# Optimization experiments

Measured on AMD Instinct MI355X. Metric: run time of the kernel, lower is better.

The kernel has to match this reference:

```python
import jax, jax.numpy as jnp
import numpy as np

D = 256        # d_model
NH = 8         # num_head
NL = 4         # num_level
KS = 8         # kernel_size (even)
K2 = KS * KS
HD = D // NH   # head_dim
LEVELS = [(128, 128), (64, 64), (32, 32), (16, 16)]


def _kernel_indices():
    # even kernel: linspace(-KS/2+0.5, KS/2-0.5, KS), meshgrid ij, stack [j,i] (x,y), / KS
    idx = np.linspace(-KS // 2 + 0.5, KS // 2 - 0.5, KS).astype(np.float32)
    i, j = np.meshgrid(idx, idx, indexing='ij')
    return jnp.asarray(np.stack([j, i], axis=-1).reshape(-1, 2) / KS)  # [K2, 2]


def setup_inputs():
    key = jax.random.key(0)
    ks = jax.random.split(key, 12)
    b, q = 2, 300
    l2 = sum(h * w for h, w in LEVELS)
    query = jax.random.normal(ks[0], (b, q, D), jnp.float32)
    value = jax.random.normal(ks[1], (b, l2, D), jnp.float32)
    v_shape = np.array(LEVELS, dtype=np.int64)                      # [NL, 2] (H, W)
    starts = np.concatenate([[0], np.cumsum([h * w for h, w in LEVELS])[:-1]])
    v_start_index = starts.astype(np.int64)                          # [NL]
    v_mask = jnp.zeros((b, l2), dtype=bool)                          # no padding
    v_valid_ratios = jnp.ones((b, 1, 1, NL, 1, 2), jnp.float32)
    center = jax.random.uniform(ks[2], (b, q, 2), jnp.float32, 0.25, 0.75)
    size = jax.random.uniform(ks[3], (b, q, 2), jnp.float32, 0.05, 0.25)
    ref_windows = jnp.concatenate([center, size], axis=-1)           # [b, q, 4] cx,cy,w,h
    s = 0.02
    Wv = s * jax.random.normal(ks[4], (D, D), jnp.float32)
    bv = jnp.zeros((D,), jnp.float32)
    Wbox = s * jax.random.normal(ks[5], (NH * NL * 4, D), jnp.float32)
    bbox = jax.random.uniform(ks[6], (NH * NL * 4,), jnp.float32)    # uniform init per _reset_parameters
    Wattn = s * jax.random.normal(ks[7], (NH * NL * 4, D), jnp.float32)
    battn = s * jax.random.normal(ks[8], (NH * NL * 4,), jnp.float32)
    Wout = s * jax.random.normal(ks[9], (D, D), jnp.float32)
    bout = jnp.zeros((D,), jnp.float32)
    return dict(query=query, value=value, v_shape=v_shape, v_mask=v_mask,
                v_start_index=v_start_index, v_valid_ratios=v_valid_ratios,
                ref_windows=ref_windows, Wv=Wv, bv=bv, Wbox=Wbox, bbox=bbox,
                Wattn=Wattn, battn=battn, Wout=Wout, bout=bout,
                kernel_indices=_kernel_indices())


def reference(query, value, v_shape, v_mask, v_start_index, v_valid_ratios,
              ref_windows, Wv, bv, Wbox, bbox, Wattn, battn, Wout, bout,
              kernel_indices):
    b, q, _ = query.shape
    # value projection + mask fill
    val = jnp.einsum('bnd,ed->bne', value, Wv) + bv
    val = jnp.where(v_mask[..., None], 0.0, val)
    val = val.reshape(b, -1, NH, HD)                                 # [b, l2, NH, HD]

    # attention logits: base 2x2 grid expanded to KSxKS via repeat_interleave
    aw = (jnp.einsum('bqd,od->bqo', query, Wattn) + battn).reshape(b, q, NH, NL, 2, 2)
    aw = jnp.repeat(jnp.repeat(aw, KS // 2, axis=-1), KS // 2, axis=-2)  # [b,q,NH,NL,KS,KS]
    spatial = jax.nn.softmax(aw.reshape(b, q, NH, NL * K2), axis=-1).reshape(b, q, NH, NL, K2)
    level = jax.nn.softmax(aw, axis=3).reshape(b, q, NH, NL, K2)

    # sampling grid (_where_to_attend)
    ob = (jnp.einsum('bqd,od->bqo', query, Wbox) + bbox).reshape(b, q, NH, NL, 4)
    rw = ref_windows[:, :, None, None, :]                            # [b,q,1,1,4]
    boxes = rw + ob / 8.0 * rw[..., jnp.array([2, 3, 2, 3])]
    center = boxes[..., None, :2]                                    # [b,q,NH,NL,1,2]
    size = boxes[..., None, 2:]
    grid = center + kernel_indices * jax.nn.relu(size)               # [b,q,NH,NL,K2,2]
    grid = grid * v_valid_ratios

    # multi-level bilinear sampling (grid_sample, align_corners=False, zero padding)
    bi = jnp.arange(b)[:, None, None, None]
    hi = jnp.arange(NH)[None, None, :, None]
    sampled = []
    for lv in range(NL):
        Hl = int(v_shape[lv, 0]); Wl = int(v_shape[lv, 1]); st = int(v_start_index[lv])
        vl = val[:, st:st + Hl * Wl]                                 # [b, Hl*Wl, NH, HD]
        loc = grid[:, :, :, lv]                                      # [b,q,NH,K2,2]
        x = loc[..., 0] * Wl - 0.5
        y = loc[..., 1] * Hl - 0.5
        x0 = jnp.floor(x); y0 = jnp.floor(y)
        dx = x - x0; dy = y - y0
        acc = jnp.zeros((b, q, NH, K2, HD), val.dtype)
        for ix, iy, w in ((x0, y0, (1 - dx) * (1 - dy)),
                          (x0 + 1, y0, dx * (1 - dy)),
                          (x0, y0 + 1, (1 - dx) * dy),
                          (x0 + 1, y0 + 1, dx * dy)):
            valid = (ix >= 0) & (ix < Wl) & (iy >= 0) & (iy < Hl)
            idx = (jnp.clip(iy, 0, Hl - 1) * Wl + jnp.clip(ix, 0, Wl - 1)).astype(jnp.int32)
            v4 = vl[bi, idx, hi]                                     # [b,q,NH,K2,HD]
            acc = acc + jnp.where(valid, w, 0.0)[..., None] * v4
        sampled.append(acc)
    sampled = jnp.stack(sampled, axis=3)                             # [b,q,NH,NL,K2,HD]

    # box-attention output: spatial softmax over all (level, point)
    out = jnp.einsum('bqhlkd,bqhlk->bqhd', sampled, spatial).reshape(b, q, D)
    out = jnp.einsum('bqd,od->bqo', out, Wout) + bout
    # instance mask output: level softmax per kernel point
    mask = jnp.einsum('bqhlkd,bqhlk->bqkhd', sampled, level).reshape(b, q, K2, D)
    mask = jnp.einsum('bqkd,od->bqko', mask, Wout) + bout
    return out, mask
```

## Files before the change

kernel.cpp:

```cpp
#include <hip/hip_runtime.h>
#include <cstdint>
#include <cstddef>

typedef unsigned short u16;
typedef unsigned int   u32;
typedef __attribute__((ext_vector_type(8))) short bf16x8;
typedef __attribute__((ext_vector_type(4))) float f32x4;

static constexpr int kQ = 300;
static constexpr int kL2 = 21760;

__device__ __forceinline__ u16 bf16_rne(float f) {
    u32 u = __float_as_uint(f);
    u += 0x7FFFu + ((u >> 16) & 1u);
    return (u16)(u >> 16);
}
__device__ __forceinline__ u32 pack2(float lo, float hi) {
    return (u32)bf16_rne(lo) | ((u32)bf16_rne(hi) << 16);
}
__device__ __forceinline__ float lo16(u32 u) { return __uint_as_float(u << 16); }
__device__ __forceinline__ float hi16(u32 u) { return __uint_as_float(u & 0xFFFF0000u); }

__global__ __launch_bounds__(256)
void f32_to_bf16(const float* __restrict__ src, u16* __restrict__ dst, int n)
{
    int i = (blockIdx.x * 256 + threadIdx.x) * 8;
    if (i >= n) return;
    float4 a = *(const float4*)(src + i);
    float4 b = *(const float4*)(src + i + 4);
    uint4 o;
    o.x = pack2(a.x, a.y); o.y = pack2(a.z, a.w);
    o.z = pack2(b.x, b.y); o.w = pack2(b.z, b.w);
    *(uint4*)(dst + i) = o;
}

template<bool OUT_BF16>
__global__ __launch_bounds__(256)
void gemm_bf16(const u16* __restrict__ A, const u16* __restrict__ W,
               const float* __restrict__ bias, void* __restrict__ Cout,
               const unsigned char* __restrict__ rowmask)
{
    __shared__ u16 S[8192];
    u16* As = S;
    u16* Bs = S + 4096;
    const int tid = threadIdx.x;
    const int m0 = blockIdx.x * 128;
    const int n0 = blockIdx.y * 128;
    const int lane = tid & 63;
    const int w = tid >> 6;
    const int wm = w & 1, wn = w >> 1;
    const int g = lane >> 4, r = lane & 15;

    f32x4 acc[4][4];
#pragma unroll
    for (int i = 0; i < 4; i++)
#pragma unroll
        for (int j = 0; j < 4; j++)
            acc[i][j] = (f32x4){0.f, 0.f, 0.f, 0.f};

    for (int kt = 0; kt < 8; ++kt) {
        const int k0 = kt * 32;
#pragma unroll
        for (int i = 0; i < 2; ++i) {
            int c = tid + i * 256;
            int m = c >> 2, gg = c & 3;
            uint4 va = *(const uint4*)(A + (size_t)(m0 + m) * 256 + k0 + gg * 8);
            *(uint4*)(As + ((gg * 128 + m) << 3)) = va;
            uint4 vb = *(const uint4*)(W + (size_t)(n0 + m) * 256 + k0 + gg * 8);
            *(uint4*)(Bs + ((gg * 128 + m) << 3)) = vb;
        }
        __syncthreads();
        bf16x8 af[4], bf[4];
#pragma unroll
        for (int mf = 0; mf < 4; ++mf)
            af[mf] = *(const bf16x8*)(As + ((g * 128 + wm * 64 + mf * 16 + r) << 3));
#pragma unroll
        for (int nf = 0; nf < 4; ++nf)
            bf[nf] = *(const bf16x8*)(Bs + ((g * 128 + wn * 64 + nf * 16 + r) << 3));
#pragma unroll
        for (int mf = 0; mf < 4; ++mf)
#pragma unroll
            for (int nf = 0; nf < 4; ++nf)
                acc[mf][nf] = __builtin_amdgcn_mfma_f32_16x16x32_bf16(
                    af[mf], bf[nf], acc[mf][nf], 0, 0, 0);
        __syncthreads();
    }

    if (!OUT_BF16) {
        float* C = (float*)Cout;
#pragma unroll
        for (int nf = 0; nf < 4; ++nf) {
            int ng = n0 + wn * 64 + nf * 16 + r;
            float bb = bias[ng];
#pragma unroll
            for (int mf = 0; mf < 4; ++mf) {
                int mg = m0 + wm * 64 + mf * 16 + g * 4;
#pragma unroll
                for (int reg = 0; reg < 4; ++reg) {
                    float z = 1.f;
                    if (rowmask && rowmask[mg + reg]) z = 0.f;
                    C[(size_t)(mg + reg) * 256 + ng] = (acc[mf][nf][reg] + bb) * z;
                }
            }
        }
    } else {
        u16* C = (u16*)Cout;
#pragma unroll
        for (int round = 0; round < 2; ++round) {
            __syncthreads();
            if (wn == round) {
#pragma unroll
                for (int nf = 0; nf < 4; ++nf) {
                    int col = nf * 16 + r;
                    float bb = bias[n0 + round * 64 + col];
#pragma unroll
                    for (int mf = 0; mf < 4; ++mf) {
                        int row0 = wm * 64 + mf * 16 + g * 4;
#pragma unroll
                        for (int reg = 0; reg < 4; ++reg) {
                            float z = 1.f;
                            if (rowmask && rowmask[m0 + row0 + reg]) z = 0.f;
                            S[(row0 + reg) * 64 + col] =
                                bf16_rne((acc[mf][nf][reg] + bb) * z);
                        }
                    }
                }
            }
            __syncthreads();
            int row = tid >> 1, hb = tid & 1;
            const u16* src = S + row * 64 + hb * 32;
            u16* dst = C + (size_t)(m0 + row) * 256 + n0 + round * 64 + hb * 32;
#pragma unroll
            for (int j = 0; j < 4; ++j)
                ((uint4*)dst)[j] = ((const uint4*)src)[j];
        }
    }
}

__global__ __launch_bounds__(256)
void gemm_nt_bias(const float* __restrict__ A, const float* __restrict__ W,
                  const float* __restrict__ bias, float* __restrict__ C, int M)
{
    __shared__ float As[32][68];
    __shared__ float Ws[32][68];
    const int tid = threadIdx.x;
    const int m0 = blockIdx.x * 64;
    const int n0 = blockIdx.y * 64;
    const int tx = tid & 15, ty = tid >> 4;
    float acc[4][4] = {};

    for (int k0 = 0; k0 < 256; k0 += 32) {
#pragma unroll
        for (int i = 0; i < 2; i++) {
            int t = tid + i * 256;
            int rr = t >> 3;
            int c4 = (t & 7) << 2;
            int ra = min(m0 + rr, M - 1);
            float4 va = *(const float4*)(A + (size_t)ra * 256 + k0 + c4);
            As[c4 + 0][rr] = va.x; As[c4 + 1][rr] = va.y;
            As[c4 + 2][rr] = va.z; As[c4 + 3][rr] = va.w;
            float4 vw = *(const float4*)(W + (size_t)(n0 + rr) * 256 + k0 + c4);
            Ws[c4 + 0][rr] = vw.x; Ws[c4 + 1][rr] = vw.y;
            Ws[c4 + 2][rr] = vw.z; Ws[c4 + 3][rr] = vw.w;
        }
        __syncthreads();
#pragma unroll
        for (int kk = 0; kk < 32; kk++) {
            float4 a = *(const float4*)&As[kk][ty * 4];
            float4 wv4 = *(const float4*)&Ws[kk][tx * 4];
            float av[4] = {a.x, a.y, a.z, a.w};
            float wv[4] = {wv4.x, wv4.y, wv4.z, wv4.w};
#pragma unroll
            for (int i = 0; i < 4; i++)
#pragma unroll
                for (int j = 0; j < 4; j++)
                    acc[i][j] += av[i] * wv[j];
        }
        __syncthreads();
    }
#pragma unroll
    for (int i = 0; i < 4; i++) {
        int rr = m0 + ty * 4 + i;
        if (rr >= M) continue;
        int n = n0 + tx * 4;
        float4 o;
        o.x = acc[i][0] + bias[n + 0];
        o.y = acc[i][1] + bias[n + 1];
        o.z = acc[i][2] + bias[n + 2];
        o.w = acc[i][3] + bias[n + 3];
        *(float4*)(C + (size_t)rr * 256 + n) = o;
    }
}

__global__ __launch_bounds__(256)
void param_kernel(const float* __restrict__ query,
                  const float* __restrict__ Wattn, const float* __restrict__ battn,
                  const float* __restrict__ Wbox,  const float* __restrict__ bbox,
                  const float* __restrict__ ref_windows,
                  const float* __restrict__ vvr,
                  float* __restrict__ params)
{
    __shared__ float qrow[256];
    __shared__ float awob[256];
    __shared__ float4 boxs[8][4];
    __shared__ float wgts[8][4][4];
    __shared__ float cqds[8][4];

    const int bq = blockIdx.x;
    const int b = bq / kQ;
    const int tid = threadIdx.x;

    if (tid < 64)
        ((float4*)qrow)[tid] = ((const float4*)(query + (size_t)bq * 256))[tid];
    __syncthreads();

    {
        const float* Wrow = (tid < 128) ? (Wattn + (size_t)tid * 256)
                                        : (Wbox + (size_t)(tid - 128) * 256);
        float s = (tid < 128) ? battn[tid] : bbox[tid - 128];
#pragma unroll 8
        for (int d4 = 0; d4 < 64; d4++) {
            float4 wv = ((const float4*)Wrow)[d4];
            float4 qv = ((const float4*)qrow)[d4];
            s += wv.x * qv.x + wv.y * qv.y + wv.z * qv.z + wv.w * qv.w;
        }
        awob[tid] = s;
    }
    __syncthreads();

    if (tid < 8) {
        const int h = tid;
        float m = -1e30f;
        float E[16];
#pragma unroll
        for (int i = 0; i < 16; i++) m = fmaxf(m, awob[h * 16 + i]);
        float Ssum = 0.f;
#pragma unroll
        for (int i = 0; i < 16; i++) { E[i] = expf(awob[h * 16 + i] - m); Ssum += E[i]; }
        float invS16 = 1.f / (16.f * Ssum);
#pragma unroll
        for (int qd = 0; qd < 4; qd++) {
            float Sq = E[qd] + E[4 + qd] + E[8 + qd] + E[12 + qd];
            float inv = 1.f / Sq;
#pragma unroll
            for (int l = 0; l < 4; l++) wgts[h][l][qd] = E[l * 4 + qd] * inv;
            cqds[h][qd] = Sq * invS16;
        }
    }
    if (tid >= 64 && tid < 96) {
        const int t = tid - 64;
        const int h = t >> 2, l = t & 3;
        float4 rw = ((const float4*)ref_windows)[bq];
        float ob0 = awob[128 + h * 16 + l * 4 + 0];
        float ob1 = awob[128 + h * 16 + l * 4 + 1];
        float ob2 = awob[128 + h * 16 + l * 4 + 2];
        float ob3 = awob[128 + h * 16 + l * 4 + 3];
        float cx = rw.x + ob0 * 0.125f * rw.z;
        float cy = rw.y + ob1 * 0.125f * rw.w;
        float sx = fmaxf(rw.z + ob2 * 0.125f * rw.z, 0.f);
        float sy = fmaxf(rw.w + ob3 * 0.125f * rw.w, 0.f);
        float vrx = vvr[(b * 4 + l) * 2 + 0];
        float vry = vvr[(b * 4 + l) * 2 + 1];
        boxs[h][l] = make_float4(cx * vrx, cy * vry, sx * vrx, sy * vry);
    }
    __syncthreads();

    float* p = params + (size_t)bq * 288;
    if (tid < 32)       ((float4*)p)[tid] = ((float4*)boxs)[tid];
    else if (tid < 64)  ((float4*)p)[tid] = ((float4*)wgts)[tid - 32];
    else if (tid < 72)  ((float4*)p)[tid] = ((float4*)cqds)[tid - 64];
}

__global__ __launch_bounds__(512)
void sample_bf16(const u16* __restrict__ valb,
                 const float* __restrict__ params,
                 u16* __restrict__ maskb,
                 float* __restrict__ out_part)
{
    __shared__ float4 boxs[8][4];
    __shared__ float wgts[8][4][4];
    __shared__ float cqds[8][4];
    __shared__ float warr[8][256];

    const int blk = blockIdx.x;
    const int bq = blk >> 2;
    const int kq = blk & 3;
    const int b = bq / kQ;
    const int tid = threadIdx.x;

    if (tid < 72) {
        float4 v = ((const float4*)(params + (size_t)bq * 288))[tid];
        if (tid < 32)      ((float4*)boxs)[tid] = v;
        else if (tid < 64) ((float4*)wgts)[tid - 32] = v;
        else               ((float4*)cqds)[tid - 64] = v;
    }
    __syncthreads();

    const int klocal = tid >> 5;
    const int h = (tid >> 2) & 7;
    const int ch = tid & 3;
    const int k = kq * 16 + klocal;
    const float kx = (float)(k & 7) * 0.125f - 0.4375f;
    const float ky = (float)(k >> 3) * 0.125f - 0.4375f;
    const int qd = (((k >> 5) & 1) << 1) | ((k >> 2) & 1);

    float acc[8];
#pragma unroll
    for (int e = 0; e < 8; e++) acc[e] = 0.f;

    static constexpr int LW[4]  = {128, 64, 32, 16};
    static constexpr int LST[4] = {0, 16384, 20480, 21504};

#pragma unroll
    for (int l = 0; l < 4; l++) {
        const int Wl = LW[l];
        const u16* vbase = valb + ((size_t)(b * kL2 + LST[l]) << 8) + h * 32 + ch * 8;
        float4 bx = boxs[h][l];
        float lw = wgts[h][l][qd];
        float x = (bx.x + kx * bx.z) * Wl - 0.5f;
        float y = (bx.y + ky * bx.w) * Wl - 0.5f;
        float x0f = floorf(x), y0f = floorf(y);
        float dx = x - x0f, dy = y - y0f;
        int x0 = (int)x0f, y0 = (int)y0f;
        int x1 = x0 + 1, y1 = y0 + 1;
        int x0c = min(max(x0, 0), Wl - 1), x1c = min(max(x1, 0), Wl - 1);
        int y0c = min(max(y0, 0), Wl - 1), y1c = min(max(y1, 0), Wl - 1);
        float vx0 = (x0 >= 0 && x0 < Wl) ? 1.f : 0.f;
        float vx1 = (x1 >= 0 && x1 < Wl) ? 1.f : 0.f;
        float vy0 = (y0 >= 0 && y0 < Wl) ? 1.f : 0.f;
        float vy1 = (y1 >= 0 && y1 < Wl) ? 1.f : 0.f;
        float w00 = (1.f - dx) * (1.f - dy) * vx0 * vy0 * lw;
        float w10 = dx * (1.f - dy) * vx1 * vy0 * lw;
        float w01 = (1.f - dx) * dy * vx0 * vy1 * lw;
        float w11 = dx * dy * vx1 * vy1 * lw;
        uint4 v00 = *(const uint4*)(vbase + ((size_t)(y0c * Wl + x0c) << 8));
        uint4 v10 = *(const uint4*)(vbase + ((size_t)(y0c * Wl + x1c) << 8));
        uint4 v01 = *(const uint4*)(vbase + ((size_t)(y1c * Wl + x0c) << 8));
        uint4 v11 = *(const uint4*)(vbase + ((size_t)(y1c * Wl + x1c) << 8));
        acc[0] += w00*lo16(v00.x) + w10*lo16(v10.x) + w01*lo16(v01.x) + w11*lo16(v11.x);
        acc[1] += w00*hi16(v00.x) + w10*hi16(v10.x) + w01*hi16(v01.x) + w11*hi16(v11.x);
        acc[2] += w00*lo16(v00.y) + w10*lo16(v10.y) + w01*lo16(v01.y) + w11*lo16(v11.y);
        acc[3] += w00*hi16(v00.y) + w10*hi16(v10.y) + w01*hi16(v01.y) + w11*hi16(v11.y);
        acc[4] += w00*lo16(v00.z) + w10*lo16(v10.z) + w01*lo16(v01.z) + w11*lo16(v11.z);
        acc[5] += w00*hi16(v00.z) + w10*hi16(v10.z) + w01*hi16(v01.z) + w11*hi16(v11.z);
        acc[6] += w00*lo16(v00.w) + w10*lo16(v10.w) + w01*lo16(v01.w) + w11*lo16(v11.w);
        acc[7] += w00*hi16(v00.w) + w10*hi16(v10.w) + w01*hi16(v01.w) + w11*hi16(v11.w);
    }

    {
        uint4 o;
        o.x = pack2(acc[0], acc[1]);
        o.y = pack2(acc[2], acc[3]);
        o.z = pack2(acc[4], acc[5]);
        o.w = pack2(acc[6], acc[7]);
        *(uint4*)(maskb + (((size_t)bq * 64 + k) << 8) + h * 32 + ch * 8) = o;
    }

    {
        const int wave = tid >> 6;
        const int lane = tid & 63;
        float c = cqds[h][qd];
#pragma unroll
        for (int e = 0; e < 8; e++) {
            float v = acc[e] * c;
            v += __shfl_xor(v, 32);
            if (lane < 32) warr[wave][h * 32 + ch * 8 + e] = v;
        }
    }
    __syncthreads();
    if (tid < 256) {
        float s = 0.f;
#pragma unroll
        for (int wv = 0; wv < 8; wv++) s += warr[wv][tid];
        out_part[(size_t)blk * 256 + tid] = s;
    }
}

__global__ __launch_bounds__(256)
void combine_kernel(const float* __restrict__ out_part, float* __restrict__ out_pre)
{
    const int bq = blockIdx.x;
    const int d = threadIdx.x;
    const float* p = out_part + (size_t)(4 * bq) * 256 + d;
    out_pre[(size_t)bq * 256 + d] = (p[0] + p[256]) + (p[512] + p[768]);
}

extern "C" void kernel_launch(void* const* d_in, const int* in_sizes, int n_in,
                              void* d_out, int out_size, void* d_ws, size_t ws_size,
                              hipStream_t stream)
{
    const float* query       = (const float*)d_in[0];
    const float* value       = (const float*)d_in[1];
    const unsigned char* v_mask = (const unsigned char*)d_in[3];
    const float* vvr         = (const float*)d_in[5];
    const float* ref_windows = (const float*)d_in[6];
    const float* Wv    = (const float*)d_in[7];
    const float* bv    = (const float*)d_in[8];
    const float* Wbox  = (const float*)d_in[9];
    const float* bbox  = (const float*)d_in[10];
    const float* Wattn = (const float*)d_in[11];
    const float* battn = (const float*)d_in[12];
    const float* Wout  = (const float*)d_in[13];
    const float* bout  = (const float*)d_in[14];

    char* wsp = (char*)d_ws;
    u16* value_b = (u16*)wsp;                 wsp += (size_t)11141120 * 2;
    u16* Wv_b    = (u16*)wsp;                 wsp += (size_t)65536 * 2;
    u16* Wout_b  = (u16*)wsp;                 wsp += (size_t)65536 * 2;
    u16* val_b   = (u16*)wsp;                 wsp += (size_t)11141120 * 2;
    u16* mask_b  = (u16*)wsp;                 wsp += (size_t)9830400 * 2;
    float* params   = (float*)wsp;            wsp += (size_t)600 * 288 * 4;
    float* out_part = (float*)wsp;            wsp += (size_t)2400 * 256 * 4;
    float* out_pre  = (float*)wsp;            wsp += (size_t)600 * 256 * 4;

    float* out  = (float*)d_out;
    float* mask = out + (size_t)600 * 256;

    f32_to_bf16<<<5440, 256, 0, stream>>>(value, value_b, 11141120);
    f32_to_bf16<<<32, 256, 0, stream>>>(Wv, Wv_b, 65536);
    f32_to_bf16<<<32, 256, 0, stream>>>(Wout, Wout_b, 65536);
    gemm_bf16<true><<<dim3(340, 2), 256, 0, stream>>>(value_b, Wv_b, bv, val_b, v_mask);
    param_kernel<<<600, 256, 0, stream>>>(query, Wattn, battn, Wbox, bbox,
                                          ref_windows, vvr, params);
    sample_bf16<<<2400, 512, 0, stream>>>(val_b, params, mask_b, out_part);
    combine_kernel<<<600, 256, 0, stream>>>(out_part, out_pre);
    gemm_bf16<false><<<dim3(300, 2), 256, 0, stream>>>(mask_b, Wout_b, bout, mask, nullptr);
    gemm_nt_bias<<<dim3(10, 4), 256, 0, stream>>>(out_pre, Wout, bout, out, 600);
}
```

Before: 138.7 us.

## Fuse value f32-to-bf16 conversion into GEMM, widen N tile, fold combine into output GEMM

The separate pass that converts the large value tensor to bf16 is removed. The value-projection GEMM now reads fp32 directly and packs to bf16 while loading its tile, which saves a full write and re-read of about 22 MB of bf16 data. The GEMM now covers all 256 output columns per block with 512 threads, so the A tile is loaded once instead of twice. The two weight conversions are merged into one launch, and the partial-sum combine kernel is folded into the A-load of the final output GEMM. The cost is more LDS per block, possibly lower occupancy, and fp32 A reads inside the GEMM loop.

```diff
diff --git a/kernel.cpp b/kernel.cpp
--- a/kernel.cpp
+++ b/kernel.cpp
@@ -22,10 +22,12 @@
 __device__ __forceinline__ float hi16(u32 u) { return __uint_as_float(u & 0xFFFF0000u); }
 
 __global__ __launch_bounds__(256)
-void f32_to_bf16(const float* __restrict__ src, u16* __restrict__ dst, int n)
-{
-    int i = (blockIdx.x * 256 + threadIdx.x) * 8;
-    if (i >= n) return;
+void convert_weights(const float* __restrict__ Wv, u16* __restrict__ Wv_b,
+                     const float* __restrict__ Wout, u16* __restrict__ Wout_b)
+{
+    const float* src = (blockIdx.x < 32) ? Wv : Wout;
+    u16* dst = (blockIdx.x < 32) ? Wv_b : Wout_b;
+    int i = ((blockIdx.x & 31) * 256 + threadIdx.x) * 8;
     float4 a = *(const float4*)(src + i);
     float4 b = *(const float4*)(src + i + 4);
     uint4 o;
@@ -34,18 +36,17 @@
     *(uint4*)(dst + i) = o;
 }
 
-template<bool OUT_BF16>
-__global__ __launch_bounds__(256)
-void gemm_bf16(const u16* __restrict__ A, const u16* __restrict__ W,
-               const float* __restrict__ bias, void* __restrict__ Cout,
-               const unsigned char* __restrict__ rowmask)
-{
-    __shared__ u16 S[8192];
+template<bool A_F32, bool OUT_BF16>
+__global__ __launch_bounds__(512)
+void gemm_bn256(const void* __restrict__ Aptr, const u16* __restrict__ W,
+                const float* __restrict__ bias, void* __restrict__ Cout,
+                const unsigned char* __restrict__ rowmask)
+{
+    __shared__ u16 S[12288];
     u16* As = S;
     u16* Bs = S + 4096;
     const int tid = threadIdx.x;
     const int m0 = blockIdx.x * 128;
-    const int n0 = blockIdx.y * 128;
     const int lane = tid & 63;
     const int w = tid >> 6;
     const int wm = w & 1, wn = w >> 1;
@@ -60,14 +61,29 @@
 
     for (int kt = 0; kt < 8; ++kt) {
         const int k0 = kt * 32;
+        {
+            int row = tid >> 2, gg = tid & 3;
+            if (A_F32) {
+                const float* A = (const float*)Aptr;
+                const float* p = A + (size_t)(m0 + row) * 256 + k0 + gg * 8;
+                float4 a0 = *(const float4*)p;
+                float4 a1 = *(const float4*)(p + 4);
+                uint4 o;
+                o.x = pack2(a0.x, a0.y); o.y = pack2(a0.z, a0.w);
+                o.z = pack2(a1.x, a1.y); o.w = pack2(a1.z, a1.w);
+                *(uint4*)(As + ((gg * 128 + row) << 3)) = o;
+            } else {
+                const u16* A = (const u16*)Aptr;
+                uint4 va = *(const uint4*)(A + (size_t)(m0 + row) * 256 + k0 + gg * 8);
+                *(uint4*)(As + ((gg * 128 + row) << 3)) = va;
+            }
+        }
 #pragma unroll
         for (int i = 0; i < 2; ++i) {
-            int c = tid + i * 256;
-            int m = c >> 2, gg = c & 3;
-            uint4 va = *(const uint4*)(A + (size_t)(m0 + m) * 256 + k0 + gg * 8);
-            *(uint4*)(As + ((gg * 128 + m) << 3)) = va;
-            uint4 vb = *(const uint4*)(W + (size_t)(n0 + m) * 256 + k0 + gg * 8);
-            *(uint4*)(Bs + ((gg * 128 + m) << 3)) = vb;
+            int c = tid + i * 512;
+            int row = c >> 2, gg = c & 3;
+            uint4 vb = *(const uint4*)(W + (size_t)row * 256 + k0 + gg * 8);
+            *(uint4*)(Bs + ((gg * 256 + row) << 3)) = vb;
         }
         __syncthreads();
         bf16x8 af[4], bf[4];
@@ -76,7 +92,7 @@
             af[mf] = *(const bf16x8*)(As + ((g * 128 + wm * 64 + mf * 16 + r) << 3));
 #pragma unroll
         for (int nf = 0; nf < 4; ++nf)
-            bf[nf] = *(const bf16x8*)(Bs + ((g * 128 + wn * 64 + nf * 16 + r) << 3));
+            bf[nf] = *(const bf16x8*)(Bs + ((g * 256 + wn * 64 + nf * 16 + r) << 3));
 #pragma unroll
         for (int mf = 0; mf < 4; ++mf)
 #pragma unroll
@@ -90,7 +106,7 @@
         float* C = (float*)Cout;
 #pragma unroll
         for (int nf = 0; nf < 4; ++nf) {
-            int ng = n0 + wn * 64 + nf * 16 + r;
+            int ng = wn * 64 + nf * 16 + r;
             float bb = bias[ng];
 #pragma unroll
             for (int mf = 0; mf < 4; ++mf) {
@@ -106,13 +122,12 @@
     } else {
         u16* C = (u16*)Cout;
 #pragma unroll
-        for (int round = 0; round < 2; ++round) {
-            __syncthreads();
+        for (int round = 0; round < 4; ++round) {
             if (wn == round) {
 #pragma unroll
                 for (int nf = 0; nf < 4; ++nf) {
                     int col = nf * 16 + r;
-                    float bb = bias[n0 + round * 64 + col];
+                    float bb = bias[round * 64 + col];
 #pragma unroll
                     for (int mf = 0; mf < 4; ++mf) {
                         int row0 = wm * 64 + mf * 16 + g * 4;
@@ -127,19 +142,21 @@
                 }
             }
             __syncthreads();
-            int row = tid >> 1, hb = tid & 1;
-            const u16* src = S + row * 64 + hb * 32;
-            u16* dst = C + (size_t)(m0 + row) * 256 + n0 + round * 64 + hb * 32;
-#pragma unroll
-            for (int j = 0; j < 4; ++j)
-                ((uint4*)dst)[j] = ((const uint4*)src)[j];
+#pragma unroll
+            for (int i = 0; i < 2; ++i) {
+                int c = tid + i * 512;
+                int row = c >> 3, cc = c & 7;
+                *(uint4*)(C + (size_t)(m0 + row) * 256 + round * 64 + cc * 8) =
+                    *(const uint4*)(S + row * 64 + cc * 8);
+            }
+            __syncthreads();
         }
     }
 }
 
 __global__ __launch_bounds__(256)
-void gemm_nt_bias(const float* __restrict__ A, const float* __restrict__ W,
-                  const float* __restrict__ bias, float* __restrict__ C, int M)
+void gemm_out_fused(const float* __restrict__ out_part, const float* __restrict__ W,
+                    const float* __restrict__ bias, float* __restrict__ C, int M)
 {
     __shared__ float As[32][68];
     __shared__ float Ws[32][68];
@@ -156,7 +173,16 @@
             int rr = t >> 3;
             int c4 = (t & 7) << 2;
             int ra = min(m0 + rr, M - 1);
-            float4 va = *(const float4*)(A + (size_t)ra * 256 + k0 + c4);
+            const float* p = out_part + (size_t)(4 * ra) * 256 + k0 + c4;
+            float4 v0 = *(const float4*)p;
+            float4 v1 = *(const float4*)(p + 256);
+            float4 v2 = *(const float4*)(p + 512);
+            float4 v3 = *(const float4*)(p + 768);
+            float4 va;
+            va.x = (v0.x + v1.x) + (v2.x + v3.x);
+            va.y = (v0.y + v1.y) + (v2.y + v3.y);
+            va.z = (v0.z + v1.z) + (v2.z + v3.z);
+            va.w = (v0.w + v1.w) + (v2.w + v3.w);
             As[c4 + 0][rr] = va.x; As[c4 + 1][rr] = va.y;
             As[c4 + 2][rr] = va.z; As[c4 + 3][rr] = va.w;
             float4 vw = *(const float4*)(W + (size_t)(n0 + rr) * 256 + k0 + c4);
@@ -376,15 +402,6 @@
     }
 }
 
-__global__ __launch_bounds__(256)
-void combine_kernel(const float* __restrict__ out_part, float* __restrict__ out_pre)
-{
-    const int bq = blockIdx.x;
-    const int d = threadIdx.x;
-    const float* p = out_part + (size_t)(4 * bq) * 256 + d;
-    out_pre[(size_t)bq * 256 + d] = (p[0] + p[256]) + (p[512] + p[768]);
-}
-
 extern "C" void kernel_launch(void* const* d_in, const int* in_sizes, int n_in,
                               void* d_out, int out_size, void* d_ws, size_t ws_size,
                               hipStream_t stream)
@@ -404,26 +421,21 @@
     const float* bout  = (const float*)d_in[14];
 
     char* wsp = (char*)d_ws;
-    u16* value_b = (u16*)wsp;                 wsp += (size_t)11141120 * 2;
     u16* Wv_b    = (u16*)wsp;                 wsp += (size_t)65536 * 2;
     u16* Wout_b  = (u16*)wsp;                 wsp += (size_t)65536 * 2;
     u16* val_b   = (u16*)wsp;                 wsp += (size_t)11141120 * 2;
     u16* mask_b  = (u16*)wsp;                 wsp += (size_t)9830400 * 2;
     float* params   = (float*)wsp;            wsp += (size_t)600 * 288 * 4;
     float* out_part = (float*)wsp;            wsp += (size_t)2400 * 256 * 4;
-    float* out_pre  = (float*)wsp;            wsp += (size_t)600 * 256 * 4;
 
     float* out  = (float*)d_out;
     float* mask = out + (size_t)600 * 256;
 
-    f32_to_bf16<<<5440, 256, 0, stream>>>(value, value_b, 11141120);
-    f32_to_bf16<<<32, 256, 0, stream>>>(Wv, Wv_b, 65536);
-    f32_to_bf16<<<32, 256, 0, stream>>>(Wout, Wout_b, 65536);
-    gemm_bf16<true><<<dim3(340, 2), 256, 0, stream>>>(value_b, Wv_b, bv, val_b, v_mask);
+    convert_weights<<<64, 256, 0, stream>>>(Wv, Wv_b, Wout, Wout_b);
     param_kernel<<<600, 256, 0, stream>>>(query, Wattn, battn, Wbox, bbox,
                                           ref_windows, vvr, params);
+    gemm_bn256<true, true><<<340, 512, 0, stream>>>(value, Wv_b, bv, val_b, v_mask);
     sample_bf16<<<2400, 512, 0, stream>>>(val_b, params, mask_b, out_part);
-    combine_kernel<<<600, 256, 0, stream>>>(out_part, out_pre);
-    gemm_bf16<false><<<dim3(300, 2), 256, 0, stream>>>(mask_b, Wout_b, bout, mask, nullptr);
-    gemm_nt_bias<<<dim3(10, 4), 256, 0, stream>>>(out_pre, Wout, bout, out, 600);
-}
+    gemm_bn256<false, false><<<300, 512, 0, stream>>>(mask_b, Wout_b, bout, mask, nullptr);
+    gemm_out_fused<<<dim3(10, 4), 256, 0, stream>>>(out_part, Wout, bout, out, 600);
+}
```

Measured after the change: 167.5 us. +20.8%, slower.
